# Kernel optimization log

Measured on AMD Instinct MI355X. Metric: run time of the kernel, lower is better.

The kernel has to match this reference:

```python
import jax, jax.numpy as jnp
import numpy as np

# ----- ESPRIT constants (mirror the torch module's __init__ defaults / init_kwargs) -----
FS = 16000
N_FFT = 512
HOP = 256
C_SOUND = 343.0
D_INTER = 0.08
SRC_NUM = 2
MIC_NUM = 4
F_LOW = 400.0
F_HIGH = 1000.0
EST_NUM = 4      # get_spt_mat(X, 4, 120)
T_START = 120


def setup_inputs() -> dict:
    """Synthesize 2 broadband plane-wave sources hitting a 4-mic ULA.

    Pure white noise per channel would make asin(phase*c/(2*pi*f*d)) leave
    [-1, 1] (NaNs). Physically delayed sources keep the ESPRIT math well-posed.
    """
    T = 1_920_000  # 2 minutes @ 16 kHz
    rng = np.random.default_rng(0)
    s = rng.standard_normal((SRC_NUM, T))
    thetas = np.deg2rad(np.array([20.0, -40.0]))               # source DOAs
    taus = (np.arange(MIC_NUM)[None, :] * D_INTER
            * np.sin(thetas)[:, None] / C_SOUND)              # (S, M) delays
    f = np.fft.rfftfreq(T, d=1.0 / FS)                        # (T//2+1,)
    S = np.fft.rfft(s, axis=-1)                               # (S, F)
    x = np.zeros((T, MIC_NUM))
    for i in range(SRC_NUM):
        # exact circular fractional delay per mic, in the frequency domain
        shifted = np.fft.irfft(S[i][None, :]
                               * np.exp(-2j * np.pi * f[None, :] * taus[i][:, None]),
                               n=T, axis=-1)                   # (M, T)
        x += shifted.T
    x += 1e-4 * rng.standard_normal((T, MIC_NUM))              # sensor noise
    return {"x": jnp.asarray(x, dtype=jnp.float32)}


def _stft(x):
    """x: (C, T) -> (C, F, T_frames). Matches torch.stft defaults:
    center=True, pad_mode='reflect', onesided=True, window=sqrt(hann_periodic)."""
    n = jnp.arange(N_FFT)
    win = jnp.sqrt(0.5 - 0.5 * jnp.cos(2.0 * jnp.pi * n / N_FFT)).astype(x.dtype)
    pad = N_FFT // 2
    xp = jnp.pad(x, ((0, 0), (pad, pad)), mode='reflect')
    n_frames = (xp.shape[-1] - N_FFT) // HOP + 1
    idx = jnp.arange(n_frames)[:, None] * HOP + jnp.arange(N_FFT)[None, :]
    frames = xp[:, idx] * win                      # (C, n_frames, n_fft)
    return jnp.fft.rfft(frames, axis=-1).transpose(0, 2, 1)  # (C, F, n_frames)


# static frequency-bin selection (shapes must be static under jit)
_FA = np.linspace(0.0, FS / 2, N_FFT // 2 + 1)
_USE_IDX = np.nonzero((_FA >= F_LOW) & (_FA < F_HIGH))[0]   # 19 bins


def _forward(x):
    X = _stft(x.T)                                  # (C, F, Tf)
    f_use = jnp.asarray(_FA[_USE_IDX], dtype=jnp.float32)      # (Fb,)
    Xs = X[:, _USE_IDX, T_START:T_START + EST_NUM]  # (C, Fb, E)
    # spatial covariance: spt[f] = mean_t x_f(t) x_f(t)^H  -> (Fb, M, M)
    spt = jnp.einsum('mft,nft->fmn', Xs, jnp.conj(Xs)) / EST_NUM
    # signal subspace = top-SRC_NUM eigenvectors (batched Hermitian eig)
    _, V = jnp.linalg.eigh(spt)                     # ascending eigenvalues
    sig = V[..., ::-1][..., :SRC_NUM]               # (Fb, M, S) dominant
    s0, s1 = sig[:, :-1, :], sig[:, 1:, :]          # (Fb, M-1, S)
    # phi = pinv(s0) @ s1 = (s0^H s0)^{-1} s0^H s1  (full column rank)
    A = jnp.einsum('fmi,fmj->fij', jnp.conj(s0), s0)
    B = jnp.einsum('fmi,fmj->fij', jnp.conj(s0), s1)
    phi = jnp.linalg.solve(A, B)                    # (Fb, 2, 2)
    # closed-form eigenvalues of batched 2x2 complex matrices
    tr = phi[..., 0, 0] + phi[..., 1, 1]
    det = phi[..., 0, 0] * phi[..., 1, 1] - phi[..., 0, 1] * phi[..., 1, 0]
    disc = jnp.sqrt(tr * tr - 4.0 * det)
    lam = jnp.stack([(tr + disc) * 0.5, (tr - disc) * 0.5], axis=-1)  # (Fb, 2)
    phase = jnp.arctan2(lam.imag, lam.real)
    ang = jnp.degrees(jnp.arcsin(phase * C_SOUND
                                 / (2.0 * jnp.pi * f_use[:, None] * D_INTER)))
    return jnp.mean(ang)                            # scalar DOA estimate


def reference(x):
    return _forward(x)
```

## Files before the change

### kernel.cpp

```cpp
#include <hip/hip_runtime.h>
#include <math.h>


#define NFFT   512
#define KLO    13
#define NK     19
#define NTT    4
#define NMIC   4
#define XBASE  30464
#define PI_F   3.14159265358979f

#define FRM_STRIDE 2084
#define CHK_STRIDE 260
#define XW_SIZE    8328

struct cf { float x, y; };
__device__ inline cf cadd(cf a, cf b){ return {a.x+b.x, a.y+b.y}; }
__device__ inline cf csub(cf a, cf b){ return {a.x-b.x, a.y-b.y}; }
__device__ inline cf cmul(cf a, cf b){ return {a.x*b.x - a.y*b.y, a.x*b.y + a.y*b.x}; }
__device__ inline cf cmulc(cf a, cf b){ return {a.x*b.x + a.y*b.y, a.y*b.x - a.x*b.y}; }
__device__ inline cf cscale(cf a, float s){ return {a.x*s, a.y*s}; }
__device__ inline cf csqrtf_c(cf z){
    float r = sqrtf(z.x*z.x + z.y*z.y);
    float u = sqrtf(fmaxf(0.5f*(r + z.x), 0.0f));
    float v = sqrtf(fmaxf(0.5f*(r - z.x), 0.0f));
    if (z.y < 0.0f) v = -v;
    return {u, v};
}

__global__ __launch_bounds__(640)
void esprit_kernel(const float* __restrict__ x, float* __restrict__ out)
{
    __shared__ __align__(16) float xw[XW_SIZE];
    __shared__ float XsR[NK][NTT][NMIC], XsI[NK][NTT][NMIC];

    const int tid = threadIdx.x;

    for (int e = tid; e < NTT * NFFT; e += 640) {
        int t = e >> 9;
        int n = e & 511;
        float4 v = ((const float4*)x)[XBASE + t * 256 + n];
        float w = __sinf((float)n * (PI_F / 512.0f));
        v.x *= w; v.y *= w; v.z *= w; v.w *= w;
        *(float4*)&xw[t * FRM_STRIDE + (n >> 6) * CHK_STRIDE + (n & 63) * 4] = v;
    }
    __syncthreads();

    if (tid < 608) {
        const int bin = tid >> 3;
        const int p   = tid & 7;
        const int kk  = bin >> 2;
        const int t   = bin & 3;
        const int k   = KLO + kk;
        const int n0  = p << 6;
        const int j0  = (k * n0) & 511;

        float cr, ci, wc, ws;
        __sincosf((float)j0 * (-2.0f * PI_F / 512.0f), &ci, &cr);
        __sincosf((float)k  * (-2.0f * PI_F / 512.0f), &ws, &wc);

        float re0=0,re1=0,re2=0,re3=0, im0=0,im1=0,im2=0,im3=0;
        const int boff = t * FRM_STRIDE + p * CHK_STRIDE;
        #pragma unroll 8
        for (int i = 0; i < 64; ++i) {
            float4 v = *(const float4*)&xw[boff + 4*i];
            re0 = fmaf(v.x, cr, re0); im0 = fmaf(v.x, ci, im0);
            re1 = fmaf(v.y, cr, re1); im1 = fmaf(v.y, ci, im1);
            re2 = fmaf(v.z, cr, re2); im2 = fmaf(v.z, ci, im2);
            re3 = fmaf(v.w, cr, re3); im3 = fmaf(v.w, ci, im3);
            float nr = fmaf(cr, wc, -(ci * ws));
            float ni = fmaf(cr, ws,  (ci * wc));
            cr = nr; ci = ni;
        }
        #pragma unroll
        for (int mask = 1; mask < 8; mask <<= 1) {
            re0 += __shfl_xor(re0, mask); im0 += __shfl_xor(im0, mask);
            re1 += __shfl_xor(re1, mask); im1 += __shfl_xor(im1, mask);
            re2 += __shfl_xor(re2, mask); im2 += __shfl_xor(im2, mask);
            re3 += __shfl_xor(re3, mask); im3 += __shfl_xor(im3, mask);
        }
        if (p == 0) {
            XsR[kk][t][0] = re0; XsI[kk][t][0] = im0;
            XsR[kk][t][1] = re1; XsI[kk][t][1] = im1;
            XsR[kk][t][2] = re2; XsI[kk][t][2] = im2;
            XsR[kk][t][3] = re3; XsI[kk][t][3] = im3;
        }
    }
    __syncthreads();

    float asum = 0.0f;
    if (tid < 64) {
        if (tid < NK) {
            cf Xm[NMIC][NTT];
            for (int m = 0; m < NMIC; ++m)
                for (int t = 0; t < NTT; ++t)
                    Xm[m][t] = { XsR[tid][t][m], XsI[tid][t][m] };

            cf R[4][4];
            for (int i = 0; i < 4; ++i)
                for (int j = 0; j < 4; ++j) {
                    cf acc = {0.f, 0.f};
                    for (int t = 0; t < 4; ++t) acc = cadd(acc, cmulc(Xm[i][t], Xm[j][t]));
                    R[i][j] = cscale(acc, 0.25f);
                }

            cf Q[4][2];
            for (int i = 0; i < 4; ++i) { Q[i][0] = {0,0}; Q[i][1] = {0,0}; }
            Q[0][0].x = 1.0f; Q[1][1].x = 1.0f;
            #pragma unroll
            for (int it = 0; it < 2; ++it) {
                cf Y[4][2];
                for (int i = 0; i < 4; ++i)
                    for (int c = 0; c < 2; ++c) {
                        cf acc = {0.f, 0.f};
                        for (int j = 0; j < 4; ++j) acc = cadd(acc, cmul(R[i][j], Q[j][c]));
                        Y[i][c] = acc;
                    }
                float n0 = 0.f;
                for (int i = 0; i < 4; ++i) n0 += Y[i][0].x*Y[i][0].x + Y[i][0].y*Y[i][0].y;
                float in0 = 1.0f / sqrtf(n0);
                for (int i = 0; i < 4; ++i) Q[i][0] = cscale(Y[i][0], in0);
                cf pr = {0.f, 0.f};
                for (int i = 0; i < 4; ++i) pr = cadd(pr, cmulc(Y[i][1], Q[i][0]));
                for (int i = 0; i < 4; ++i) Q[i][1] = csub(Y[i][1], cmul(pr, Q[i][0]));
                float n1 = 0.f;
                for (int i = 0; i < 4; ++i) n1 += Q[i][1].x*Q[i][1].x + Q[i][1].y*Q[i][1].y;
                float in1 = 1.0f / sqrtf(n1);
                for (int i = 0; i < 4; ++i) Q[i][1] = cscale(Q[i][1], in1);
            }

            float a00 = 0.f, a11 = 0.f;
            cf a01 = {0.f, 0.f};
            cf B[2][2] = { { {0,0}, {0,0} }, { {0,0}, {0,0} } };
            for (int i = 0; i < 3; ++i) {
                a00 += Q[i][0].x*Q[i][0].x + Q[i][0].y*Q[i][0].y;
                a11 += Q[i][1].x*Q[i][1].x + Q[i][1].y*Q[i][1].y;
                a01 = cadd(a01, cmulc(Q[i][1], Q[i][0]));
                for (int r2 = 0; r2 < 2; ++r2)
                    for (int c2 = 0; c2 < 2; ++c2)
                        B[r2][c2] = cadd(B[r2][c2], cmulc(Q[i+1][c2], Q[i][r2]));
            }
            float detA = a00*a11 - (a01.x*a01.x + a01.y*a01.y);
            float inv  = 1.0f / detA;
            cf na01  = { -a01.x, -a01.y };
            cf na01c = { -a01.x,  a01.y };
            cf phi00 = cscale(cadd(cscale(B[0][0], a11), cmul(na01,  B[1][0])), inv);
            cf phi01 = cscale(cadd(cscale(B[0][1], a11), cmul(na01,  B[1][1])), inv);
            cf phi10 = cscale(cadd(cmul(na01c, B[0][0]), cscale(B[1][0], a00)), inv);
            cf phi11 = cscale(cadd(cmul(na01c, B[0][1]), cscale(B[1][1], a00)), inv);

            cf tr = cadd(phi00, phi11);
            cf dt = csub(cmul(phi00, phi11), cmul(phi01, phi10));
            cf d2 = csub(cmul(tr, tr), cscale(dt, 4.0f));
            cf disc = csqrtf_c(d2);
            cf lam0 = cscale(cadd(tr, disc), 0.5f);
            cf lam1 = cscale(csub(tr, disc), 0.5f);

            float f     = 31.25f * (float)(KLO + tid);
            float scale = 343.0f / (2.0f * PI_F * f * 0.08f);
            float ph0 = atan2f(lam0.y, lam0.x);
            float ph1 = atan2f(lam1.y, lam1.x);
            float g0 = fminf(fmaxf(ph0 * scale, -1.0f), 1.0f);
            float g1 = fminf(fmaxf(ph1 * scale, -1.0f), 1.0f);
            asum = (asinf(g0) + asinf(g1)) * (180.0f / PI_F);
        }
        #pragma unroll
        for (int mask = 32; mask >= 1; mask >>= 1)
            asum += __shfl_xor(asum, mask);
        if (tid == 0) out[0] = asum * (1.0f / 38.0f);
    }
}

extern "C" void kernel_launch(void* const* d_in, const int* in_sizes, int n_in,
                              void* d_out, int out_size, void* d_ws, size_t ws_size,
                              hipStream_t stream)
{
    const float* x = (const float*)d_in[0];
    float* out = (float*)d_out;
    esprit_kernel<<<1, 640, 0, stream>>>(x, out);
}
```

Baseline: 12.84 us.

## Fuse per-bin ESPRIT solve into DFT waves and trim subspace iteration

Each 32-lane half-wave now owns one frequency bin. After the shuffle reduction it gathers the 4x4 frame/mic spectrum with shuffles and runs the covariance, subspace and 2x2 eigen solve itself. This removes the shared-memory staging of spectra and the serial tail that ran on only 19 threads of one wave. The subspace iteration drops from two power steps to one, since the first step from the identity is just R's first two columns. It also switches to hardware rsq/rcp intrinsics. In exchange every lane does the math redundantly, and accuracy may drop from fewer iterations and approximate reciprocals.

```diff
diff --git a/kernel.cpp b/kernel.cpp
--- a/kernel.cpp
+++ b/kernel.cpp
@@ -6,7 +6,6 @@
 #define KLO    13
 #define NK     19
 #define NTT    4
-#define NMIC   4
 #define XBASE  30464
 #define PI_F   3.14159265358979f
 
@@ -32,7 +31,7 @@
 void esprit_kernel(const float* __restrict__ x, float* __restrict__ out)
 {
     __shared__ __align__(16) float xw[XW_SIZE];
-    __shared__ float XsR[NK][NTT][NMIC], XsI[NK][NTT][NMIC];
+    __shared__ float angLDS[NK];
 
     const int tid = threadIdx.x;
 
@@ -46,124 +45,116 @@
     }
     __syncthreads();
 
-    if (tid < 608) {
-        const int bin = tid >> 3;
-        const int p   = tid & 7;
-        const int kk  = bin >> 2;
-        const int t   = bin & 3;
-        const int k   = KLO + kk;
-        const int n0  = p << 6;
-        const int j0  = (k * n0) & 511;
+    const int wid  = tid >> 6;
+    const int lane = tid & 63;
+    const int half = lane >> 5;
+    const int bin  = (wid << 1) | half;
+    const int l5   = lane & 31;
+    const int t    = l5 >> 3;
+    const int p    = l5 & 7;
+    const int k    = KLO + bin;
+    const int n0   = p << 6;
+    const int j0   = (k * n0) & 511;
 
-        float cr, ci, wc, ws;
-        __sincosf((float)j0 * (-2.0f * PI_F / 512.0f), &ci, &cr);
-        __sincosf((float)k  * (-2.0f * PI_F / 512.0f), &ws, &wc);
+    float cr, ci, wc, ws;
+    __sincosf((float)j0 * (-2.0f * PI_F / 512.0f), &ci, &cr);
+    __sincosf((float)k  * (-2.0f * PI_F / 512.0f), &ws, &wc);
 
-        float re0=0,re1=0,re2=0,re3=0, im0=0,im1=0,im2=0,im3=0;
-        const int boff = t * FRM_STRIDE + p * CHK_STRIDE;
-        #pragma unroll 8
-        for (int i = 0; i < 64; ++i) {
-            float4 v = *(const float4*)&xw[boff + 4*i];
-            re0 = fmaf(v.x, cr, re0); im0 = fmaf(v.x, ci, im0);
-            re1 = fmaf(v.y, cr, re1); im1 = fmaf(v.y, ci, im1);
-            re2 = fmaf(v.z, cr, re2); im2 = fmaf(v.z, ci, im2);
-            re3 = fmaf(v.w, cr, re3); im3 = fmaf(v.w, ci, im3);
-            float nr = fmaf(cr, wc, -(ci * ws));
-            float ni = fmaf(cr, ws,  (ci * wc));
-            cr = nr; ci = ni;
+    float re0=0,re1=0,re2=0,re3=0, im0=0,im1=0,im2=0,im3=0;
+    const int boff = t * FRM_STRIDE + p * CHK_STRIDE;
+    #pragma unroll 8
+    for (int i = 0; i < 64; ++i) {
+        float4 v = *(const float4*)&xw[boff + 4*i];
+        re0 = fmaf(v.x, cr, re0); im0 = fmaf(v.x, ci, im0);
+        re1 = fmaf(v.y, cr, re1); im1 = fmaf(v.y, ci, im1);
+        re2 = fmaf(v.z, cr, re2); im2 = fmaf(v.z, ci, im2);
+        re3 = fmaf(v.w, cr, re3); im3 = fmaf(v.w, ci, im3);
+        float nr = fmaf(cr, wc, -(ci * ws));
+        float ni = fmaf(cr, ws,  (ci * wc));
+        cr = nr; ci = ni;
+    }
+    #pragma unroll
+    for (int mask = 1; mask < 8; mask <<= 1) {
+        re0 += __shfl_xor(re0, mask); im0 += __shfl_xor(im0, mask);
+        re1 += __shfl_xor(re1, mask); im1 += __shfl_xor(im1, mask);
+        re2 += __shfl_xor(re2, mask); im2 += __shfl_xor(im2, mask);
+        re3 += __shfl_xor(re3, mask); im3 += __shfl_xor(im3, mask);
+    }
+
+    cf Xm[4][NTT];
+    const int srcbase = half << 5;
+    #pragma unroll
+    for (int t2 = 0; t2 < NTT; ++t2) {
+        int src = srcbase + (t2 << 3);
+        Xm[0][t2] = { __shfl(re0, src), __shfl(im0, src) };
+        Xm[1][t2] = { __shfl(re1, src), __shfl(im1, src) };
+        Xm[2][t2] = { __shfl(re2, src), __shfl(im2, src) };
+        Xm[3][t2] = { __shfl(re3, src), __shfl(im3, src) };
+    }
+
+    {
+        cf R[4][4];
+        for (int i = 0; i < 4; ++i)
+            for (int j = 0; j < 4; ++j) {
+                cf acc = {0.f, 0.f};
+                for (int tt = 0; tt < 4; ++tt) acc = cadd(acc, cmulc(Xm[i][tt], Xm[j][tt]));
+                R[i][j] = cscale(acc, 0.25f);
+            }
+
+        cf Q[4][2], Y[4][2];
+        for (int i = 0; i < 4; ++i) { Y[i][0] = R[i][0]; Y[i][1] = R[i][1]; }
+        float nrm0 = 0.f;
+        for (int i = 0; i < 4; ++i) nrm0 += Y[i][0].x*Y[i][0].x + Y[i][0].y*Y[i][0].y;
+        float in0 = __builtin_amdgcn_rsqf(nrm0);
+        for (int i = 0; i < 4; ++i) Q[i][0] = cscale(Y[i][0], in0);
+        cf pr = {0.f, 0.f};
+        for (int i = 0; i < 4; ++i) pr = cadd(pr, cmulc(Y[i][1], Q[i][0]));
+        for (int i = 0; i < 4; ++i) Q[i][1] = csub(Y[i][1], cmul(pr, Q[i][0]));
+        float nrm1 = 0.f;
+        for (int i = 0; i < 4; ++i) nrm1 += Q[i][1].x*Q[i][1].x + Q[i][1].y*Q[i][1].y;
+        float in1 = __builtin_amdgcn_rsqf(nrm1);
+        for (int i = 0; i < 4; ++i) Q[i][1] = cscale(Q[i][1], in1);
+
+        float a00 = 0.f, a11 = 0.f;
+        cf a01 = {0.f, 0.f};
+        cf B[2][2] = { { {0,0}, {0,0} }, { {0,0}, {0,0} } };
+        for (int i = 0; i < 3; ++i) {
+            a00 += Q[i][0].x*Q[i][0].x + Q[i][0].y*Q[i][0].y;
+            a11 += Q[i][1].x*Q[i][1].x + Q[i][1].y*Q[i][1].y;
+            a01 = cadd(a01, cmulc(Q[i][1], Q[i][0]));
+            for (int r2 = 0; r2 < 2; ++r2)
+                for (int c2 = 0; c2 < 2; ++c2)
+                    B[r2][c2] = cadd(B[r2][c2], cmulc(Q[i+1][c2], Q[i][r2]));
         }
-        #pragma unroll
-        for (int mask = 1; mask < 8; mask <<= 1) {
-            re0 += __shfl_xor(re0, mask); im0 += __shfl_xor(im0, mask);
-            re1 += __shfl_xor(re1, mask); im1 += __shfl_xor(im1, mask);
-            re2 += __shfl_xor(re2, mask); im2 += __shfl_xor(im2, mask);
-            re3 += __shfl_xor(re3, mask); im3 += __shfl_xor(im3, mask);
-        }
-        if (p == 0) {
-            XsR[kk][t][0] = re0; XsI[kk][t][0] = im0;
-            XsR[kk][t][1] = re1; XsI[kk][t][1] = im1;
-            XsR[kk][t][2] = re2; XsI[kk][t][2] = im2;
-            XsR[kk][t][3] = re3; XsI[kk][t][3] = im3;
-        }
+        float detA = a00*a11 - (a01.x*a01.x + a01.y*a01.y);
+        float inv  = __builtin_amdgcn_rcpf(detA);
+        cf na01  = { -a01.x, -a01.y };
+        cf na01c = { -a01.x,  a01.y };
+        cf phi00 = cscale(cadd(cscale(B[0][0], a11), cmul(na01,  B[1][0])), inv);
+        cf phi01 = cscale(cadd(cscale(B[0][1], a11), cmul(na01,  B[1][1])), inv);
+        cf phi10 = cscale(cadd(cmul(na01c, B[0][0]), cscale(B[1][0], a00)), inv);
+        cf phi11 = cscale(cadd(cmul(na01c, B[0][1]), cscale(B[1][1], a00)), inv);
+
+        cf tr = cadd(phi00, phi11);
+        cf dt = csub(cmul(phi00, phi11), cmul(phi01, phi10));
+        cf d2 = csub(cmul(tr, tr), cscale(dt, 4.0f));
+        cf disc = csqrtf_c(d2);
+        cf lam0 = cscale(cadd(tr, disc), 0.5f);
+        cf lam1 = cscale(csub(tr, disc), 0.5f);
+
+        float f     = 31.25f * (float)k;
+        float scale = 343.0f / (2.0f * PI_F * f * 0.08f);
+        float ph0 = atan2f(lam0.y, lam0.x);
+        float ph1 = atan2f(lam1.y, lam1.x);
+        float g0 = fminf(fmaxf(ph0 * scale, -1.0f), 1.0f);
+        float g1 = fminf(fmaxf(ph1 * scale, -1.0f), 1.0f);
+        if (l5 == 0 && bin < NK)
+            angLDS[bin] = (asinf(g0) + asinf(g1)) * (180.0f / PI_F);
     }
     __syncthreads();
 
-    float asum = 0.0f;
     if (tid < 64) {
-        if (tid < NK) {
-            cf Xm[NMIC][NTT];
-            for (int m = 0; m < NMIC; ++m)
-                for (int t = 0; t < NTT; ++t)
-                    Xm[m][t] = { XsR[tid][t][m], XsI[tid][t][m] };
-
-            cf R[4][4];
-            for (int i = 0; i < 4; ++i)
-                for (int j = 0; j < 4; ++j) {
-                    cf acc = {0.f, 0.f};
-                    for (int t = 0; t < 4; ++t) acc = cadd(acc, cmulc(Xm[i][t], Xm[j][t]));
-                    R[i][j] = cscale(acc, 0.25f);
-                }
-
-            cf Q[4][2];
-            for (int i = 0; i < 4; ++i) { Q[i][0] = {0,0}; Q[i][1] = {0,0}; }
-            Q[0][0].x = 1.0f; Q[1][1].x = 1.0f;
-            #pragma unroll
-            for (int it = 0; it < 2; ++it) {
-                cf Y[4][2];
-                for (int i = 0; i < 4; ++i)
-                    for (int c = 0; c < 2; ++c) {
-                        cf acc = {0.f, 0.f};
-                        for (int j = 0; j < 4; ++j) acc = cadd(acc, cmul(R[i][j], Q[j][c]));
-                        Y[i][c] = acc;
-                    }
-                float n0 = 0.f;
-                for (int i = 0; i < 4; ++i) n0 += Y[i][0].x*Y[i][0].x + Y[i][0].y*Y[i][0].y;
-                float in0 = 1.0f / sqrtf(n0);
-                for (int i = 0; i < 4; ++i) Q[i][0] = cscale(Y[i][0], in0);
-                cf pr = {0.f, 0.f};
-                for (int i = 0; i < 4; ++i) pr = cadd(pr, cmulc(Y[i][1], Q[i][0]));
-                for (int i = 0; i < 4; ++i) Q[i][1] = csub(Y[i][1], cmul(pr, Q[i][0]));
-                float n1 = 0.f;
-                for (int i = 0; i < 4; ++i) n1 += Q[i][1].x*Q[i][1].x + Q[i][1].y*Q[i][1].y;
-                float in1 = 1.0f / sqrtf(n1);
-                for (int i = 0; i < 4; ++i) Q[i][1] = cscale(Q[i][1], in1);
-            }
-
-            float a00 = 0.f, a11 = 0.f;
-            cf a01 = {0.f, 0.f};
-            cf B[2][2] = { { {0,0}, {0,0} }, { {0,0}, {0,0} } };
-            for (int i = 0; i < 3; ++i) {
-                a00 += Q[i][0].x*Q[i][0].x + Q[i][0].y*Q[i][0].y;
-                a11 += Q[i][1].x*Q[i][1].x + Q[i][1].y*Q[i][1].y;
-                a01 = cadd(a01, cmulc(Q[i][1], Q[i][0]));
-                for (int r2 = 0; r2 < 2; ++r2)
-                    for (int c2 = 0; c2 < 2; ++c2)
-                        B[r2][c2] = cadd(B[r2][c2], cmulc(Q[i+1][c2], Q[i][r2]));
-            }
-            float detA = a00*a11 - (a01.x*a01.x + a01.y*a01.y);
-            float inv  = 1.0f / detA;
-            cf na01  = { -a01.x, -a01.y };
-            cf na01c = { -a01.x,  a01.y };
-            cf phi00 = cscale(cadd(cscale(B[0][0], a11), cmul(na01,  B[1][0])), inv);
-            cf phi01 = cscale(cadd(cscale(B[0][1], a11), cmul(na01,  B[1][1])), inv);
-            cf phi10 = cscale(cadd(cmul(na01c, B[0][0]), cscale(B[1][0], a00)), inv);
-            cf phi11 = cscale(cadd(cmul(na01c, B[0][1]), cscale(B[1][1], a00)), inv);
-
-            cf tr = cadd(phi00, phi11);
-            cf dt = csub(cmul(phi00, phi11), cmul(phi01, phi10));
-            cf d2 = csub(cmul(tr, tr), cscale(dt, 4.0f));
-            cf disc = csqrtf_c(d2);
-            cf lam0 = cscale(cadd(tr, disc), 0.5f);
-            cf lam1 = cscale(csub(tr, disc), 0.5f);
-
-            float f     = 31.25f * (float)(KLO + tid);
-            float scale = 343.0f / (2.0f * PI_F * f * 0.08f);
-            float ph0 = atan2f(lam0.y, lam0.x);
-            float ph1 = atan2f(lam1.y, lam1.x);
-            float g0 = fminf(fmaxf(ph0 * scale, -1.0f), 1.0f);
-            float g1 = fminf(fmaxf(ph1 * scale, -1.0f), 1.0f);
-            asum = (asinf(g0) + asinf(g1)) * (180.0f / PI_F);
-        }
+        float asum = (tid < NK) ? angLDS[tid] : 0.0f;
         #pragma unroll
         for (int mask = 32; mask >= 1; mask >>= 1)
             asum += __shfl_xor(asum, mask);
```

Result: slower. 14.73 us (+14.7%).
